# Kernel tuning notes

Measured on AMD Instinct MI355X. Metric: run time of the kernel, lower is better.

## Reference

```python
import jax, jax.numpy as jnp
import numpy as np

TOKENS = 16384
HIDDEN = 2048
GROUP_SIZE = 128
EPS = 1e-05
FP8_MAX = 448.0  # float8_e4m3fn max


def rmsnorm(x, w, eps=EPS):
    # vLLM RMSNorm: x * rsqrt(mean(x^2)) * weight
    var = jnp.mean(x * x, axis=-1, keepdims=True)
    return x * jax.lax.rsqrt(var + eps) * w


def fused_add_rmsnorm(x, residual, w, eps=EPS):
    # vLLM RMSNorm(x, residual): residual += x; out = rmsnorm(residual)
    resid = x + residual
    return rmsnorm(resid, w, eps), resid


def per_token_group_quant_fp8_ue8m0(y, group_size=GROUP_SIZE):
    # QuantFP8(static=False, group_shape=(1,128), use_ue8m0=True)
    t, h = y.shape
    g = y.reshape(t, h // group_size, group_size)
    amax = jnp.max(jnp.abs(g), axis=-1)                      # [T, H/G]
    scale = jnp.maximum(amax, 1e-10) / FP8_MAX
    scale = jnp.exp2(jnp.ceil(jnp.log2(scale)))              # ue8m0: round scale up to power of 2
    q = jnp.clip(g / scale[..., None], -FP8_MAX, FP8_MAX)
    q = q.astype(jnp.float8_e4m3fn)                          # fp8 rounding
    return q.reshape(t, h), scale


def setup_inputs() -> dict:
    key = jax.random.key(0)
    kx, kw = jax.random.split(key)
    x = jax.random.normal(kx, (TOKENS, HIDDEN), dtype=jnp.float32)
    norm_w = jnp.ones((4, HIDDEN), dtype=jnp.float32)
    w = jax.random.uniform(kw, (3, HIDDEN, HIDDEN), dtype=jnp.float32)
    return {"x": x, "norm_w": norm_w, "w": w}


def reference(x, norm_w, w):
    # tensor_model_parallel_all_reduce == identity at world_size 1
    z = jax.nn.relu(x)
    xr = z
    resid = z
    y = rmsnorm(xr, norm_w[0])
    x2 = y @ w[0]
    y2, resid = fused_add_rmsnorm(x2, resid, norm_w[1])
    y2_q, y2_s = per_token_group_quant_fp8_ue8m0(y2)
    x3 = y2_q.astype(x.dtype) @ w[1]
    y3, resid = fused_add_rmsnorm(x3, resid, norm_w[2])
    y3_q, y3_s = per_token_group_quant_fp8_ue8m0(y3)
    x4 = y3_q.astype(x.dtype) @ w[2]
    y4, resid = fused_add_rmsnorm(x4, resid, norm_w[3])
    return (y4, y2_s, y3_s)
```

## Files before the change

### kernel.cpp

```cpp
#include <hip/hip_runtime.h>
#include <stdint.h>
#include <math.h>

#define NTOK 16384
#define HID  2048
#define NGRP 16
#define EPSF 1e-5f

typedef __bf16 bf16;
typedef __bf16 bf16x8 __attribute__((ext_vector_type(8)));
typedef float  f32x4  __attribute__((ext_vector_type(4)));


__device__ __forceinline__ void async_load16(const void* g, void* l) {
  __builtin_amdgcn_global_load_lds((const __attribute__((address_space(1))) void*)g,
                                   (__attribute__((address_space(3))) void*)l, 16, 0, 0);
}

__device__ __forceinline__ void bar() {
  asm volatile("" ::: "memory");
  __builtin_amdgcn_s_barrier();
  asm volatile("" ::: "memory");
}

__device__ __forceinline__ float fp8_e4m3_rne(float v) {
  float a = fabsf(v);
  float s = (v < 0.f) ? -1.f : 1.f;
  if (a < 0.015625f) {
    float r = rintf(a * 512.0f);
    return s * r * 0.001953125f;
  }
  uint32_t u = __float_as_uint(a);
  u = (u + 0x7FFFFu + ((u >> 20) & 1u)) & 0xFFF00000u;
  return s * __uint_as_float(u);
}

__device__ __forceinline__ float block_sum256(float v) {
  __shared__ float sh[4];
  #pragma unroll
  for (int o = 32; o > 0; o >>= 1) v += __shfl_xor(v, o, 64);
  if ((threadIdx.x & 63) == 0) sh[threadIdx.x >> 6] = v;
  __syncthreads();
  return sh[0] + sh[1] + sh[2] + sh[3];
}

__device__ __forceinline__ float ue8m0_scale(float amax) {
  float v = fmaxf(amax, 1e-10f) / 448.0f;
  float l = (float)log2((double)v);
  return exp2f(ceilf(l));
}


__global__ __launch_bounds__(256) void k_transpose_cast(const float* __restrict__ W,
                                                        bf16* __restrict__ Wt) {
  __shared__ float tile[64][65];
  const size_t mat = (size_t)HID * HID;
  const float* Wz = W + mat * blockIdx.z;
  bf16* Wtz = Wt + mat * blockIdx.z;
  int bn = blockIdx.x * 64;
  int bk = blockIdx.y * 64;
  int t = threadIdx.x;
  {
    int r = t >> 4, c = (t & 15) * 4;
    #pragma unroll
    for (int i = 0; i < 4; i++) {
      float4 v = *(const float4*)(Wz + (size_t)(bk + r + 16 * i) * HID + bn + c);
      tile[r + 16 * i][c] = v.x; tile[r + 16 * i][c + 1] = v.y;
      tile[r + 16 * i][c + 2] = v.z; tile[r + 16 * i][c + 3] = v.w;
    }
  }
  __syncthreads();
  {
    int n = t >> 2, kc = (t & 3) * 16;
    bf16x8 o0, o1;
    #pragma unroll
    for (int j = 0; j < 8; j++) o0[j] = (bf16)tile[kc + j][n];
    #pragma unroll
    for (int j = 0; j < 8; j++) o1[j] = (bf16)tile[kc + 8 + j][n];
    bf16* dst = Wtz + (size_t)(bn + n) * HID + bk + kc;
    *(bf16x8*)dst = o0;
    *(bf16x8*)(dst + 8) = o1;
  }
}

__global__ __launch_bounds__(256) void k_pre(const float* __restrict__ x,
                                             const float* __restrict__ nw,
                                             bf16* __restrict__ Y,
                                             bf16* __restrict__ R) {
  size_t base = (size_t)blockIdx.x * HID + threadIdx.x * 8;
  float4 v0 = *(const float4*)(x + base);
  float4 v1 = *(const float4*)(x + base + 4);
  float z[8] = {v0.x, v0.y, v0.z, v0.w, v1.x, v1.y, v1.z, v1.w};
  float ss = 0.f;
  #pragma unroll
  for (int i = 0; i < 8; i++) { z[i] = fmaxf(z[i], 0.f); ss += z[i] * z[i]; }
  float tot = block_sum256(ss);
  float s = rsqrtf(tot * (1.0f / HID) + EPSF);
  bf16x8 rr;
  #pragma unroll
  for (int i = 0; i < 8; i++) rr[i] = (bf16)z[i];
  *(bf16x8*)(R + base) = rr;
  int j0 = threadIdx.x * 8;
  float4 w0 = *(const float4*)(nw + j0);
  float4 w1 = *(const float4*)(nw + j0 + 4);
  float wv[8] = {w0.x, w0.y, w0.z, w0.w, w1.x, w1.y, w1.z, w1.w};
  bf16x8 o;
  #pragma unroll
  for (int i = 0; i < 8; i++) o[i] = (bf16)(z[i] * s * wv[i]);
  *(bf16x8*)(Y + base) = o;
}

__global__ __launch_bounds__(256) void k_fuse_quant(const bf16* __restrict__ residIn,
                                                    const bf16* __restrict__ Cin,
                                                    const float* __restrict__ nw,
                                                    bf16* __restrict__ residOut,
                                                    bf16* __restrict__ Aout,
                                                    float* __restrict__ scaleOut) {
  int row = blockIdx.x;
  int j0 = threadIdx.x * 8;
  size_t base = (size_t)row * HID + j0;
  bf16x8 c  = *(const bf16x8*)(Cin + base);
  bf16x8 rv = *(const bf16x8*)(residIn + base);
  float r[8]; float ss = 0.f;
  #pragma unroll
  for (int i = 0; i < 8; i++) { r[i] = (float)rv[i] + (float)c[i]; ss += r[i] * r[i]; }
  float tot = block_sum256(ss);
  float s = rsqrtf(tot * (1.0f / HID) + EPSF);

  bf16x8 ro;
  #pragma unroll
  for (int i = 0; i < 8; i++) ro[i] = (bf16)r[i];
  *(bf16x8*)(residOut + base) = ro;

  float4 w0 = *(const float4*)(nw + j0);
  float4 w1 = *(const float4*)(nw + j0 + 4);
  float wv[8] = {w0.x, w0.y, w0.z, w0.w, w1.x, w1.y, w1.z, w1.w};
  float y[8], amax = 0.f;
  #pragma unroll
  for (int i = 0; i < 8; i++) { y[i] = r[i] * s * wv[i]; amax = fmaxf(amax, fabsf(y[i])); }
  amax = fmaxf(amax, __shfl_xor(amax, 1, 64));
  amax = fmaxf(amax, __shfl_xor(amax, 2, 64));
  amax = fmaxf(amax, __shfl_xor(amax, 4, 64));
  amax = fmaxf(amax, __shfl_xor(amax, 8, 64));
  float scale = ue8m0_scale(amax);
  float inv = 1.0f / scale;
  bf16x8 q;
  #pragma unroll
  for (int i = 0; i < 8; i++) {
    float t = fminf(fmaxf(y[i] * inv, -448.f), 448.f);
    q[i] = (bf16)fp8_e4m3_rne(t);
  }
  *(bf16x8*)(Aout + base) = q;
  if ((threadIdx.x & 15) == 0) scaleOut[(size_t)row * NGRP + (j0 >> 7)] = scale;
}

__global__ __launch_bounds__(256) void k_final(const bf16* __restrict__ residIn,
                                               const bf16* __restrict__ Cin,
                                               const float* __restrict__ nw,
                                               float* __restrict__ out) {
  size_t base = (size_t)blockIdx.x * HID + threadIdx.x * 8;
  bf16x8 c  = *(const bf16x8*)(Cin + base);
  bf16x8 rv = *(const bf16x8*)(residIn + base);
  float r[8]; float ss = 0.f;
  #pragma unroll
  for (int i = 0; i < 8; i++) { r[i] = (float)rv[i] + (float)c[i]; ss += r[i] * r[i]; }
  float tot = block_sum256(ss);
  float s = rsqrtf(tot * (1.0f / HID) + EPSF);
  int j0 = threadIdx.x * 8;
  float4 w0 = *(const float4*)(nw + j0);
  float4 w1 = *(const float4*)(nw + j0 + 4);
  float wv[8] = {w0.x, w0.y, w0.z, w0.w, w1.x, w1.y, w1.z, w1.w};
  float4 o0, o1;
  o0.x = r[0]*s*wv[0]; o0.y = r[1]*s*wv[1]; o0.z = r[2]*s*wv[2]; o0.w = r[3]*s*wv[3];
  o1.x = r[4]*s*wv[4]; o1.y = r[5]*s*wv[5]; o1.z = r[6]*s*wv[6]; o1.w = r[7]*s*wv[7];
  *(float4*)(out + base) = o0;
  *(float4*)(out + base + 4) = o1;
}

__global__ __launch_bounds__(512, 2) void k_gemm(const bf16* __restrict__ A,
                                                 const bf16* __restrict__ B,
                                                 bf16* __restrict__ C,
                                                 int M, int N, int K) {
  __shared__ __align__(16) char lds[4 * 32768];
  int b = blockIdx.x;
  int bn = b & 7;
  int bm = b >> 3;
  int tid = threadIdx.x;
  int wave = tid >> 6, lane = tid & 63;
  int q = lane >> 4, rr = lane & 15;
  int wm = wave >> 2, wn = wave & 3;

  const bf16* aSrc[2]; const bf16* bSrc[2];
  #pragma unroll
  for (int i = 0; i < 2; i++) {
    int m = i * 512 + tid;
    int r = m >> 2;
    int c = (m & 3) ^ ((r >> 1) & 3);
    aSrc[i] = A + (size_t)(bm * 256 + r) * K + c * 8;
    bSrc[i] = B + (size_t)(bn * 256 + r) * K + c * 8;
  }

  const int swz = (rr >> 1) & 3;
  const int ldoff = rr * 64 + ((q ^ swz) << 4);

  f32x4 acc[8][4];
  #pragma unroll
  for (int mf = 0; mf < 8; mf++)
    #pragma unroll
    for (int nf = 0; nf < 4; nf++)
      #pragma unroll
      for (int e = 0; e < 4; e++) acc[mf][nf][e] = 0.f;

  const int NT = K / 32;

  #pragma unroll
  for (int t = 0; t < 3; ++t) {
    char* db = lds + t * 32768 + wave * 1024;
    async_load16(aSrc[0] + t * 32, db);
    async_load16(aSrc[1] + t * 32, db + 8192);
    async_load16(bSrc[0] + t * 32, db + 16384);
    async_load16(bSrc[1] + t * 32, db + 16384 + 8192);
  }
  asm volatile("s_waitcnt vmcnt(8)" ::: "memory");
  bar();

  for (int t = 0; t < NT; ++t) {
    const char* sb  = lds + (t & 3) * 32768;
    const char* rbA = sb + wm * 8192 + ldoff;
    const char* rbB = sb + 16384 + wn * 4096 + ldoff;
    const int u  = (t + 3 < NT) ? (t + 3) : (NT - 1);
    char* ub = lds + ((t + 3) & 3) * 32768 + wave * 1024;

    bf16x8 bfr[4], afr[4];
    #pragma unroll
    for (int nf = 0; nf < 4; nf++)
      bfr[nf] = *(const bf16x8*)(rbB + nf * 1024);
    #pragma unroll
    for (int mf = 0; mf < 4; mf++)
      afr[mf] = *(const bf16x8*)(rbA + mf * 1024);
    async_load16(aSrc[0] + u * 32, ub);
    async_load16(aSrc[1] + u * 32, ub + 8192);
    bar();
    __builtin_amdgcn_s_setprio(1);
    #pragma unroll
    for (int mf = 0; mf < 4; mf++)
      #pragma unroll
      for (int nf = 0; nf < 4; nf++)
        acc[mf][nf] = __builtin_amdgcn_mfma_f32_16x16x32_bf16(afr[mf], bfr[nf], acc[mf][nf], 0, 0, 0);
    __builtin_amdgcn_s_setprio(0);
    bar();

    #pragma unroll
    for (int mf = 0; mf < 4; mf++)
      afr[mf] = *(const bf16x8*)(rbA + 4096 + mf * 1024);
    async_load16(bSrc[0] + u * 32, ub + 16384);
    async_load16(bSrc[1] + u * 32, ub + 16384 + 8192);
    bar();
    __builtin_amdgcn_s_setprio(1);
    #pragma unroll
    for (int mf = 0; mf < 4; mf++)
      #pragma unroll
      for (int nf = 0; nf < 4; nf++)
        acc[4 + mf][nf] = __builtin_amdgcn_mfma_f32_16x16x32_bf16(afr[mf], bfr[nf], acc[4 + mf][nf], 0, 0, 0);
    __builtin_amdgcn_s_setprio(0);
    asm volatile("s_waitcnt vmcnt(8)" ::: "memory");
    bar();
  }

  asm volatile("s_waitcnt vmcnt(0)" ::: "memory");

  #pragma unroll
  for (int mf = 0; mf < 8; mf++)
    #pragma unroll
    for (int nf = 0; nf < 4; nf++)
      #pragma unroll
      for (int tt = 0; tt < 4; tt++) {
        int rowi = bm * 256 + wm * 128 + mf * 16 + q * 4 + tt;
        int coli = bn * 256 + wn * 64 + nf * 16 + rr;
        C[(size_t)rowi * N + coli] = (bf16)acc[mf][nf][tt];
      }
}


extern "C" void kernel_launch(void* const* d_in, const int* in_sizes, int n_in,
                              void* d_out, int out_size, void* d_ws, size_t ws_size,
                              hipStream_t stream) {
  const float* x      = (const float*)d_in[0];
  const float* norm_w = (const float*)d_in[1];
  const float* w      = (const float*)d_in[2];

  float* out   = (float*)d_out;
  float* y4o   = out;
  float* s2o   = out + (size_t)NTOK * HID;
  float* s3o   = s2o + (size_t)NTOK * NGRP;

  char* ws = (char*)d_ws;
  const size_t WT_B = (size_t)3 * HID * HID * 2;
  const size_t AB_B = (size_t)NTOK * HID * 2;
  bf16* Wt   = (bf16*)ws;
  bf16* Abuf = (bf16*)(ws + WT_B);
  bf16* Cbuf = (bf16*)(ws + WT_B + AB_B);
  bf16* Rbuf = (bf16*)(ws + WT_B + 2 * AB_B);
  const size_t MATE = (size_t)HID * HID;

  dim3 gT(HID / 64, HID / 64, 3);
  int  gG = (NTOK / 256) * (HID / 256);

  k_transpose_cast<<<gT, 256, 0, stream>>>(w, Wt);
  k_pre<<<NTOK, 256, 0, stream>>>(x, norm_w, Abuf, Rbuf);
  k_gemm<<<gG, 512, 0, stream>>>(Abuf, Wt, Cbuf, NTOK, HID, HID);
  k_fuse_quant<<<NTOK, 256, 0, stream>>>(Rbuf, Cbuf, norm_w + HID, Rbuf, Abuf, s2o);
  k_gemm<<<gG, 512, 0, stream>>>(Abuf, Wt + MATE, Cbuf, NTOK, HID, HID);
  k_fuse_quant<<<NTOK, 256, 0, stream>>>(Rbuf, Cbuf, norm_w + 2 * HID, Rbuf, Abuf, s3o);
  k_gemm<<<gG, 512, 0, stream>>>(Abuf, Wt + 2 * MATE, Cbuf, NTOK, HID, HID);
  k_final<<<NTOK, 256, 0, stream>>>(Rbuf, Cbuf, norm_w + 3 * HID, y4o);
}
```

Measured before the change: 788.8 us.

## Double-buffer LDS fragments in registers and cut barriers per K-tile in GEMM

Restructures the GEMM main loop so the A/B fragments for the next K-tile are read from LDS into a second register set while the second half of the current tile's MFMAs run. Iterations are manually unrolled by two to ping-pong the register sets. All four async global-to-LDS loads are issued at the top of the tile, and barriers drop from four to two per tile. This aims to hide LDS read latency and barrier overhead behind MFMA work, at the cost of more VGPRs and tighter reliance on correct buffer reuse ordering. Reading tile t+1 right after the first barrier assumes its LDS data has already landed.

```diff
diff --git a/kernel.cpp b/kernel.cpp
--- a/kernel.cpp
+++ b/kernel.cpp
@@ -15,12 +15,6 @@
 __device__ __forceinline__ void async_load16(const void* g, void* l) {
   __builtin_amdgcn_global_load_lds((const __attribute__((address_space(1))) void*)g,
                                    (__attribute__((address_space(3))) void*)l, 16, 0, 0);
-}
-
-__device__ __forceinline__ void bar() {
-  asm volatile("" ::: "memory");
-  __builtin_amdgcn_s_barrier();
-  asm volatile("" ::: "memory");
 }
 
 __device__ __forceinline__ float fp8_e4m3_rne(float v) {
@@ -222,50 +216,68 @@
     async_load16(bSrc[1] + t * 32, db + 16384 + 8192);
   }
   asm volatile("s_waitcnt vmcnt(8)" ::: "memory");
-  bar();
-
-  for (int t = 0; t < NT; ++t) {
-    const char* sb  = lds + (t & 3) * 32768;
-    const char* rbA = sb + wm * 8192 + ldoff;
-    const char* rbB = sb + 16384 + wn * 4096 + ldoff;
-    const int u  = (t + 3 < NT) ? (t + 3) : (NT - 1);
-    char* ub = lds + ((t + 3) & 3) * 32768 + wave * 1024;
-
-    bf16x8 bfr[4], afr[4];
-    #pragma unroll
-    for (int nf = 0; nf < 4; nf++)
-      bfr[nf] = *(const bf16x8*)(rbB + nf * 1024);
-    #pragma unroll
-    for (int mf = 0; mf < 4; mf++)
-      afr[mf] = *(const bf16x8*)(rbA + mf * 1024);
-    async_load16(aSrc[0] + u * 32, ub);
-    async_load16(aSrc[1] + u * 32, ub + 8192);
-    bar();
-    __builtin_amdgcn_s_setprio(1);
-    #pragma unroll
-    for (int mf = 0; mf < 4; mf++)
-      #pragma unroll
-      for (int nf = 0; nf < 4; nf++)
-        acc[mf][nf] = __builtin_amdgcn_mfma_f32_16x16x32_bf16(afr[mf], bfr[nf], acc[mf][nf], 0, 0, 0);
-    __builtin_amdgcn_s_setprio(0);
-    bar();
-
-    #pragma unroll
-    for (int mf = 0; mf < 4; mf++)
-      afr[mf] = *(const bf16x8*)(rbA + 4096 + mf * 1024);
-    async_load16(bSrc[0] + u * 32, ub + 16384);
-    async_load16(bSrc[1] + u * 32, ub + 16384 + 8192);
-    bar();
-    __builtin_amdgcn_s_setprio(1);
-    #pragma unroll
-    for (int mf = 0; mf < 4; mf++)
-      #pragma unroll
-      for (int nf = 0; nf < 4; nf++)
-        acc[4 + mf][nf] = __builtin_amdgcn_mfma_f32_16x16x32_bf16(afr[mf], bfr[nf], acc[4 + mf][nf], 0, 0, 0);
-    __builtin_amdgcn_s_setprio(0);
-    asm volatile("s_waitcnt vmcnt(8)" ::: "memory");
-    bar();
-  }
+  asm volatile("s_barrier" ::: "memory");
+
+  bf16x8 fA[4], fB[4], gA[4], gB[4];
+  {
+    const char* rbA = lds + wm * 8192 + ldoff;
+    const char* rbB = lds + 16384 + wn * 4096 + ldoff;
+    #pragma unroll
+    for (int nf = 0; nf < 4; nf++) fB[nf] = *(const bf16x8*)(rbB + nf * 1024);
+    #pragma unroll
+    for (int mf = 0; mf < 4; mf++) fA[mf] = *(const bf16x8*)(rbA + mf * 1024);
+  }
+
+#define TILE_BODY(T, CA, CB, NA, NB)                                           \
+  {                                                                            \
+    const int t_ = (T);                                                        \
+    const char* sb_  = lds + (t_ & 3) * 32768;                                 \
+    const char* rbA_ = sb_ + wm * 8192 + ldoff;                                \
+    const int u_ = (t_ + 3 < NT) ? (t_ + 3) : (NT - 1);                        \
+    char* ub_ = lds + ((t_ + 3) & 3) * 32768 + wave * 1024;                    \
+         \
+    async_load16(aSrc[0] + u_ * 32, ub_);                                      \
+    async_load16(aSrc[1] + u_ * 32, ub_ + 8192);                               \
+    async_load16(bSrc[0] + u_ * 32, ub_ + 16384);                              \
+    async_load16(bSrc[1] + u_ * 32, ub_ + 16384 + 8192);                       \
+    bf16x8 a1_[4];                                                             \
+    _Pragma("unroll")                                                          \
+    for (int mf = 0; mf < 4; mf++)                                             \
+      a1_[mf] = *(const bf16x8*)(rbA_ + 4096 + mf * 1024);                     \
+    asm volatile("s_waitcnt vmcnt(8)" ::: "memory");      \
+    asm volatile("s_barrier" ::: "memory");                                    \
+    __builtin_amdgcn_s_setprio(1);                                             \
+    _Pragma("unroll")                                                          \
+    for (int mf = 0; mf < 4; mf++)                                             \
+      _Pragma("unroll")                                                        \
+      for (int nf = 0; nf < 4; nf++)                                           \
+        acc[mf][nf] = __builtin_amdgcn_mfma_f32_16x16x32_bf16(CA[mf], CB[nf],  \
+                                                       acc[mf][nf], 0, 0, 0);  \
+    __builtin_amdgcn_s_setprio(0);                                             \
+               \
+    const char* nb_  = lds + ((t_ + 1) & 3) * 32768;                           \
+    const char* nAp_ = nb_ + wm * 8192 + ldoff;                                \
+    const char* nBp_ = nb_ + 16384 + wn * 4096 + ldoff;                        \
+    _Pragma("unroll")                                                          \
+    for (int nf = 0; nf < 4; nf++) NB[nf] = *(const bf16x8*)(nBp_ + nf * 1024);\
+    _Pragma("unroll")                                                          \
+    for (int mf = 0; mf < 4; mf++) NA[mf] = *(const bf16x8*)(nAp_ + mf * 1024);\
+    __builtin_amdgcn_s_setprio(1);                                             \
+    _Pragma("unroll")                                                          \
+    for (int mf = 0; mf < 4; mf++)                                             \
+      _Pragma("unroll")                                                        \
+      for (int nf = 0; nf < 4; nf++)                                           \
+        acc[4 + mf][nf] = __builtin_amdgcn_mfma_f32_16x16x32_bf16(a1_[mf],     \
+                                            CB[nf], acc[4 + mf][nf], 0, 0, 0); \
+    __builtin_amdgcn_s_setprio(0);                                             \
+    asm volatile("s_barrier" ::: "memory");                                    \
+  }
+
+  for (int t = 0; t < NT; t += 2) {
+    TILE_BODY(t,     fA, fB, gA, gB)
+    TILE_BODY(t + 1, gA, gB, fA, fB)
+  }
+#undef TILE_BODY
 
   asm volatile("s_waitcnt vmcnt(0)" ::: "memory");
 
```

New measurement: 799.9 us. About the same (+1.4%).
